# Performance work log

Hardware: AMD Instinct MI355X
Metric: run time of the kernel (lower is better)

## Reference

```python
import jax, jax.numpy as jnp
import numpy as np

N_USER = 100000
N_ITEM = 50000
D = 64
E_SOC = 3200000
E_INFO = 3200000
BATCH = 16384


def setup_inputs() -> dict:
    key = jax.random.key(0)
    ks = jax.random.split(key, 8)
    return {
        "user_emb": jax.random.normal(ks[0], (N_USER, D), dtype=jnp.float32) * 0.01,
        "item_emb": jax.random.normal(ks[1], (N_ITEM, D), dtype=jnp.float32) * 0.01,
        "social_rows": jax.random.randint(ks[2], (E_SOC,), 0, N_USER, dtype=jnp.int32),
        "social_cols": jax.random.randint(ks[3], (E_SOC,), 0, N_USER, dtype=jnp.int32),
        "social_vals": jnp.ones((E_SOC,), dtype=jnp.float32),
        "info_rows": jax.random.randint(ks[4], (E_INFO,), 0, N_USER, dtype=jnp.int32),
        "info_cols": jax.random.randint(ks[5], (E_INFO,), 0, N_ITEM, dtype=jnp.int32),
        "info_vals": jnp.ones((E_INFO,), dtype=jnp.float32),
        "user_ids": jax.random.randint(ks[6], (BATCH,), 0, N_USER, dtype=jnp.int32),
        "item_ids": jax.random.randint(ks[7], (BATCH,), 0, N_ITEM, dtype=jnp.int32),
    }


def _spmm(rows, cols, vals, feats, n_rows):
    # (A @ feats) where A is COO [n_rows, n_cols]: gather, weight, scatter-add.
    msgs = vals[:, None] * feats[cols]  # [E, D]
    return jax.ops.segment_sum(msgs, rows, num_segments=n_rows)


def reference(user_emb, item_emb, social_rows, social_cols, social_vals,
              info_rows, info_cols, info_vals, user_ids, item_ids):
    n_user = user_emb.shape[0]
    eps = 1e-8

    # user embedding from items: D_info^{-1} * info_adj @ item_emb
    deg_info = jax.ops.segment_sum(info_vals, info_rows, num_segments=n_user) + eps
    user_from_items = _spmm(info_rows, info_cols, info_vals, item_emb, n_user) / deg_info[:, None]

    # two GCN layers over social graph: H' = D^{-1} A H + H
    deg_soc = jax.ops.segment_sum(social_vals, social_rows, num_segments=n_user) + eps

    def gcn(h):
        return _spmm(social_rows, social_cols, social_vals, h, n_user) / deg_soc[:, None] + h

    h1 = gcn(user_emb)
    h2 = gcn(h1)
    final_user = h1 + h2 + user_from_items

    # final_item = item_emb + init_item_feature = 2 * item_emb
    final_item = 2.0 * item_emb

    u = final_user[user_ids]
    v = final_item[item_ids]
    return jax.nn.sigmoid(jnp.sum(u * v, axis=-1))
```

## Files before the change

kernel.cpp:

```cpp
#include <hip/hip_runtime.h>
#include <hip/hip_bf16.h>

#define BA 512
#define CHUNK_A 4096
#define PB 8
#define NBINS_MAX 512
#define CAPS 8800
#define NBINM_C 64
#define CPAD 16

__device__ __forceinline__ float bf2f(unsigned short u) {
    return __uint_as_float(((unsigned int)u) << 16);
}
__device__ __forceinline__ unsigned short f2bf(float f) {
    unsigned int x = __float_as_uint(f);
    return (unsigned short)((x + 0x7fffu + ((x >> 16) & 1u)) >> 16);
}
__device__ __forceinline__ void unpk(unsigned int u, float& lo, float& hi) {
    lo = __uint_as_float(u << 16);
    hi = __uint_as_float(u & 0xffff0000u);
}
__device__ __forceinline__ unsigned int pack2(float lo, float hi) {
    return (unsigned int)f2bf(lo) | ((unsigned int)f2bf(hi) << 16);
}


__global__ __launch_bounds__(256) void conv_mark_kernel(const float* __restrict__ a,
                                                        unsigned short* __restrict__ oa, long long na,
                                                        const float* __restrict__ b,
                                                        unsigned short* __restrict__ ob, long long nb,
                                                        const float* __restrict__ sv, int Es,
                                                        const float* __restrict__ iv, int Ei,
                                                        int* __restrict__ notOnes,
                                                        const int* __restrict__ ids,
                                                        int* __restrict__ mark,
                                                        int* __restrict__ mlist,
                                                        int* __restrict__ n_marked, int n,
                                                        int* __restrict__ curS, int nbinS,
                                                        int* __restrict__ curMI, int capS) {
    long long t = (long long)blockIdx.x * blockDim.x + threadIdx.x;
    long long i4 = t * 4;
    if (i4 < na) {
        float4 f = *(const float4*)&a[i4];
        ushort4 o = { f2bf(f.x), f2bf(f.y), f2bf(f.z), f2bf(f.w) };
        *(ushort4*)&oa[i4] = o;
    }
    if (i4 < nb) {
        float4 f = *(const float4*)&b[i4];
        ushort4 o = { f2bf(f.x), f2bf(f.y), f2bf(f.z), f2bf(f.w) };
        *(ushort4*)&ob[i4] = o;
    }
    if (i4 + 4 <= Es) {
        float4 v = *(const float4*)&sv[i4];
        if (v.x != 1.f || v.y != 1.f || v.z != 1.f || v.w != 1.f) atomicOr(notOnes, 1);
    } else if (i4 < Es) {
        for (long long k = i4; k < Es; ++k) if (sv[k] != 1.f) atomicOr(notOnes, 1);
    }
    if (i4 + 4 <= Ei) {
        float4 v = *(const float4*)&iv[i4];
        if (v.x != 1.f || v.y != 1.f || v.z != 1.f || v.w != 1.f) atomicOr(notOnes, 1);
    } else if (i4 < Ei) {
        for (long long k = i4; k < Ei; ++k) if (iv[k] != 1.f) atomicOr(notOnes, 1);
    }
    int i = (int)t;
    if (i < nbinS) curS[i * CPAD] = i * capS;
    if (i < NBINM_C) curMI[i * CPAD] = i * capS;
    if (i < n) {
        int u = ids[i];
        if (atomicCAS(&mark[u], 0, -1) == 0) {
            int m = atomicAdd(n_marked, 1);
            mlist[m] = u;
            mark[u] = m + 1;
        }
    }
}

__global__ __launch_bounds__(512) void partA_all(const int* __restrict__ notOnes,
                                                 const int* __restrict__ sr,
                                                 const int* __restrict__ sc,
                                                 const float* __restrict__ sv, int Es,
                                                 const int* __restrict__ ir,
                                                 const int* __restrict__ ic,
                                                 const float* __restrict__ iv, int Ei,
                                                 const int* __restrict__ mark,
                                                 int* __restrict__ curS,
                                                 int* __restrict__ bufS4, int2* __restrict__ bufS8,
                                                 int nbinS, int capS,
                                                 int* __restrict__ curMI,
                                                 int* __restrict__ bufMI4, int2* __restrict__ bufMI8) {
    __shared__ int hS[NBINS_MAX], gS[NBINS_MAX], lS[NBINS_MAX];
    __shared__ int hI[NBINM_C], gI[NBINM_C], lI[NBINM_C];
    const bool ones = (*notOnes == 0);
    int tid = threadIdx.x;
    int base = blockIdx.x * CHUNK_A;
    for (int b = tid; b < nbinS; b += BA) hS[b] = 0;
    if (tid < NBINM_C) hI[tid] = 0;

    int e0 = base + tid * 8;
    int rS[8], cS[8], mI[8], cI[8], rI[8];
    float vS[8], vI[8];
    int nS = (e0 < Es) ? min(8, Es - e0) : 0;
    int nI = (e0 < Ei) ? min(8, Ei - e0) : 0;
    if (nS == 8) {
        *(int4*)&rS[0] = *(const int4*)&sr[e0]; *(int4*)&rS[4] = *(const int4*)&sr[e0 + 4];
        *(int4*)&cS[0] = *(const int4*)&sc[e0]; *(int4*)&cS[4] = *(const int4*)&sc[e0 + 4];
        if (!ones) {
            *(float4*)&vS[0] = *(const float4*)&sv[e0];
            *(float4*)&vS[4] = *(const float4*)&sv[e0 + 4];
        }
    } else {
        #pragma unroll 8
        for (int k = 0; k < 8; ++k)
            if (k < nS) { rS[k] = sr[e0 + k]; cS[k] = sc[e0 + k]; vS[k] = ones ? 1.f : sv[e0 + k]; }
    }
    if (nI == 8) {
        *(int4*)&rI[0] = *(const int4*)&ir[e0]; *(int4*)&rI[4] = *(const int4*)&ir[e0 + 4];
        *(int4*)&cI[0] = *(const int4*)&ic[e0]; *(int4*)&cI[4] = *(const int4*)&ic[e0 + 4];
        if (!ones) {
            *(float4*)&vI[0] = *(const float4*)&iv[e0];
            *(float4*)&vI[4] = *(const float4*)&iv[e0 + 4];
        }
    } else {
        #pragma unroll 8
        for (int k = 0; k < 8; ++k)
            if (k < nI) { rI[k] = ir[e0 + k]; cI[k] = ic[e0 + k]; vI[k] = ones ? 1.f : iv[e0 + k]; }
    }
    #pragma unroll 8
    for (int k = 0; k < 8; ++k) mI[k] = (k < nI) ? mark[rI[k]] : 0;
    __syncthreads();

    #pragma unroll 8
    for (int k = 0; k < 8; ++k) if (k < nS) atomicAdd(&hS[rS[k] >> PB], 1);
    #pragma unroll 8
    for (int k = 0; k < 8; ++k) if (mI[k] > 0) atomicAdd(&hI[(mI[k] - 1) >> 8], 1);
    __syncthreads();

    for (int b = tid; b < nbinS; b += BA) {
        int h = hS[b]; gS[b] = h ? atomicAdd(&curS[b * CPAD], h) : 0; lS[b] = 0;
    }
    if (tid < NBINM_C) {
        int h = hI[tid]; gI[tid] = h ? atomicAdd(&curMI[tid * CPAD], h) : 0; lI[tid] = 0;
    }
    __syncthreads();

    #pragma unroll 8
    for (int k = 0; k < 8; ++k) {
        if (k < nS) {
            int r = rS[k];
            int b = r >> PB;
            int off = atomicAdd(&lS[b], 1);
            long long dst = (long long)gS[b] + off;
            if (dst < (long long)(b + 1) * capS) {
                int meta = ((r & 255) << 17) | cS[k];
                if (ones) bufS4[dst] = meta;
                else      bufS8[dst] = make_int2(meta, __float_as_int(vS[k]));
            }
        }
    }
    #pragma unroll 8
    for (int k = 0; k < 8; ++k) {
        if (mI[k] > 0) {
            int m = mI[k] - 1;
            int b = m >> 8;
            int off = atomicAdd(&lI[b], 1);
            long long dst = (long long)gI[b] + off;
            if (dst < (long long)(b + 1) * capS) {
                int meta = ((m & 255) << 17) | cI[k];
                if (ones) bufMI4[dst] = meta;
                else      bufMI8[dst] = make_int2(meta, __float_as_int(vI[k]));
            }
        }
    }
}

__global__ __launch_bounds__(512) void partB_sort(const int* __restrict__ notOnes,
                                                  const int* __restrict__ cur_in,
                                                  const int* __restrict__ buf4,
                                                  const int2* __restrict__ buf8,
                                                  int* __restrict__ csr4,
                                                  int2* __restrict__ csr8,
                                                  int2* __restrict__ rowptr2,
                                                  int n_rows_total, int cap) {
    int bin = blockIdx.x;
    int rows0 = bin << 8;
    int nrows = min(256, n_rows_total - rows0);
    __shared__ int cur[256], wsum[4];
    const bool ones = (*notOnes == 0);
    int tid = threadIdx.x;
    if (tid < 256) cur[tid] = 0;
    __syncthreads();
    int gstart = bin * cap;
    int gend = cur_in[bin * CPAD];
    if (gend > gstart + cap) gend = gstart + cap;
    int cnt = gend - gstart;
    if (ones) {
        for (int i = tid; i < cnt; i += 512) atomicAdd(&cur[buf4[gstart + i] >> 17], 1);
    } else {
        for (int i = tid; i < cnt; i += 512) atomicAdd(&cur[buf8[gstart + i].x >> 17], 1);
    }
    __syncthreads();
    int lane = tid & 63, wid = tid >> 6;
    int x = 0, v = 0;
    if (tid < 256) {
        x = cur[tid]; v = x;
        #pragma unroll
        for (int d = 1; d < 64; d <<= 1) { int y = __shfl_up(v, d); if (lane >= d) v += y; }
        if (lane == 63) wsum[wid] = v;
    }
    __syncthreads();
    if (tid == 0) {
        int s = 0;
        #pragma unroll
        for (int k = 0; k < 4; ++k) { int t = wsum[k]; wsum[k] = s; s += t; }
    }
    __syncthreads();
    if (tid < 256) {
        int excl = wsum[wid] + v - x;
        if (tid < nrows) rowptr2[rows0 + tid] = make_int2(gstart + excl, gstart + excl + x);
        cur[tid] = excl;
    }
    __syncthreads();
    if (ones) {
        for (int i = tid; i < cnt; i += 512) {
            int e = buf4[gstart + i];
            int p = atomicAdd(&cur[e >> 17], 1);
            csr4[gstart + p] = e & 0x1FFFF;
        }
    } else {
        for (int i = tid; i < cnt; i += 512) {
            int2 e = buf8[gstart + i];
            int p = atomicAdd(&cur[e.x >> 17], 1);
            csr8[gstart + p] = make_int2(e.x & 0x1FFFF, e.y);
        }
    }
}

__global__ __launch_bounds__(256) void gather1_kernel(const int* __restrict__ notOnes,
                                                      const int2* __restrict__ rowptr2,
                                                      const int* __restrict__ csr4,
                                                      const int2* __restrict__ csr8,
                                                      const unsigned short* __restrict__ ub,
                                                      unsigned short* __restrict__ hb,
                                                      int n_user) {
    int w = (int)((blockIdx.x * (long long)blockDim.x + threadIdx.x) >> 6);
    if (w >= n_user) return;
    int lane = threadIdx.x & 63;
    int sub = lane >> 3;
    int d8 = (lane & 7) << 3;
    int2 seg = rowptr2[w];
    float a0 = 0, a1 = 0, a2 = 0, a3 = 0, a4 = 0, a5 = 0, a6 = 0, a7 = 0, degs;
    if (*notOnes == 0) {
        for (int j = seg.x + sub; j < seg.y; j += 8) {
            int c = csr4[j];
            int4 q = *(const int4*)&ub[(long long)c * 64 + d8];
            float f0, f1, f2, f3, f4, f5, f6, f7;
            unpk(q.x, f0, f1); unpk(q.y, f2, f3); unpk(q.z, f4, f5); unpk(q.w, f6, f7);
            a0 += f0; a1 += f1; a2 += f2; a3 += f3;
            a4 += f4; a5 += f5; a6 += f6; a7 += f7;
        }
        degs = (float)(seg.y - seg.x);
    } else {
        degs = 0.f;
        for (int j = seg.x + sub; j < seg.y; j += 8) {
            int2 e = csr8[j];
            float vv = __int_as_float(e.y);
            int4 q = *(const int4*)&ub[(long long)(e.x) * 64 + d8];
            float f0, f1, f2, f3, f4, f5, f6, f7;
            unpk(q.x, f0, f1); unpk(q.y, f2, f3); unpk(q.z, f4, f5); unpk(q.w, f6, f7);
            a0 += vv * f0; a1 += vv * f1; a2 += vv * f2; a3 += vv * f3;
            a4 += vv * f4; a5 += vv * f5; a6 += vv * f6; a7 += vv * f7;
        }
        #pragma unroll
        for (int m = 8; m < 64; m <<= 1) degs += __shfl_xor(degs, m);
    }
    #pragma unroll
    for (int m = 8; m < 64; m <<= 1) {
        a0 += __shfl_xor(a0, m); a1 += __shfl_xor(a1, m);
        a2 += __shfl_xor(a2, m); a3 += __shfl_xor(a3, m);
        a4 += __shfl_xor(a4, m); a5 += __shfl_xor(a5, m);
        a6 += __shfl_xor(a6, m); a7 += __shfl_xor(a7, m);
    }
    if (sub == 0) {
        float inv = 1.0f / (degs + 1e-8f);
        int4 qe = *(const int4*)&ub[(long long)w * 64 + d8];
        float g0, g1, g2, g3, g4, g5, g6, g7;
        unpk(qe.x, g0, g1); unpk(qe.y, g2, g3); unpk(qe.z, g4, g5); unpk(qe.w, g6, g7);
        int4 o;
        o.x = (int)pack2(fmaf(a0, inv, g0), fmaf(a1, inv, g1));
        o.y = (int)pack2(fmaf(a2, inv, g2), fmaf(a3, inv, g3));
        o.z = (int)pack2(fmaf(a4, inv, g4), fmaf(a5, inv, g5));
        o.w = (int)pack2(fmaf(a6, inv, g6), fmaf(a7, inv, g7));
        *(int4*)&hb[(long long)w * 64 + d8] = o;
    }
}

__global__ __launch_bounds__(256) void accSI_kernel(const int* __restrict__ notOnes,
                                                    const int* __restrict__ mlist,
                                                    const int* __restrict__ n_marked,
                                                    const int2* __restrict__ rowptr2,
                                                    const int* __restrict__ csrS4,
                                                    const int2* __restrict__ csrS8,
                                                    const unsigned short* __restrict__ hb,
                                                    const int2* __restrict__ rowptrI2,
                                                    const int* __restrict__ csrI4,
                                                    const int2* __restrict__ csrI8,
                                                    const unsigned short* __restrict__ ib,
                                                    float* __restrict__ accF) {
    int w = (int)((blockIdx.x * (long long)blockDim.x + threadIdx.x) >> 6);
    if (w >= *n_marked) return;
    int lane = threadIdx.x & 63;
    int sub = lane >> 3;
    int d8 = (lane & 7) << 3;
    int r = mlist[w];

    float a0 = 0, a1 = 0, a2 = 0, a3 = 0, a4 = 0, a5 = 0, a6 = 0, a7 = 0, dS;
    float b0 = 0, b1 = 0, b2 = 0, b3 = 0, b4 = 0, b5 = 0, b6 = 0, b7 = 0, dI;
    int2 segS = rowptr2[r];
    int2 segI = rowptrI2[w];
    if (*notOnes == 0) {
        for (int j = segS.x + sub; j < segS.y; j += 8) {
            int c = csrS4[j];
            int4 q = *(const int4*)&hb[(long long)c * 64 + d8];
            float f0, f1, f2, f3, f4, f5, f6, f7;
            unpk(q.x, f0, f1); unpk(q.y, f2, f3); unpk(q.z, f4, f5); unpk(q.w, f6, f7);
            a0 += f0; a1 += f1; a2 += f2; a3 += f3;
            a4 += f4; a5 += f5; a6 += f6; a7 += f7;
        }
        for (int j = segI.x + sub; j < segI.y; j += 8) {
            int c = csrI4[j];
            int4 q = *(const int4*)&ib[(long long)c * 64 + d8];
            float f0, f1, f2, f3, f4, f5, f6, f7;
            unpk(q.x, f0, f1); unpk(q.y, f2, f3); unpk(q.z, f4, f5); unpk(q.w, f6, f7);
            b0 += f0; b1 += f1; b2 += f2; b3 += f3;
            b4 += f4; b5 += f5; b6 += f6; b7 += f7;
        }
        dS = (float)(segS.y - segS.x);
        dI = (float)(segI.y - segI.x);
    } else {
        dS = 0.f; dI = 0.f;
        for (int j = segS.x + sub; j < segS.y; j += 8) {
            int2 e = csrS8[j];
            float vv = __int_as_float(e.y);
            int4 q = *(const int4*)&hb[(long long)e.x * 64 + d8];
            float f0, f1, f2, f3, f4, f5, f6, f7;
            unpk(q.x, f0, f1); unpk(q.y, f2, f3); unpk(q.z, f4, f5); unpk(q.w, f6, f7);
            a0 += vv * f0; a1 += vv * f1; a2 += vv * f2; a3 += vv * f3;
            a4 += vv * f4; a5 += vv * f5; a6 += vv * f6; a7 += vv * f7;
            dS += vv;
        }
        for (int j = segI.x + sub; j < segI.y; j += 8) {
            int2 e = csrI8[j];
            float vv = __int_as_float(e.y);
            int4 q = *(const int4*)&ib[(long long)e.x * 64 + d8];
            float f0, f1, f2, f3, f4, f5, f6, f7;
            unpk(q.x, f0, f1); unpk(q.y, f2, f3); unpk(q.z, f4, f5); unpk(q.w, f6, f7);
            b0 += vv * f0; b1 += vv * f1; b2 += vv * f2; b3 += vv * f3;
            b4 += vv * f4; b5 += vv * f5; b6 += vv * f6; b7 += vv * f7;
            dI += vv;
        }
        #pragma unroll
        for (int m = 8; m < 64; m <<= 1) { dS += __shfl_xor(dS, m); dI += __shfl_xor(dI, m); }
    }
    #pragma unroll
    for (int m = 8; m < 64; m <<= 1) {
        a0 += __shfl_xor(a0, m); a1 += __shfl_xor(a1, m);
        a2 += __shfl_xor(a2, m); a3 += __shfl_xor(a3, m);
        a4 += __shfl_xor(a4, m); a5 += __shfl_xor(a5, m);
        a6 += __shfl_xor(a6, m); a7 += __shfl_xor(a7, m);
        b0 += __shfl_xor(b0, m); b1 += __shfl_xor(b1, m);
        b2 += __shfl_xor(b2, m); b3 += __shfl_xor(b3, m);
        b4 += __shfl_xor(b4, m); b5 += __shfl_xor(b5, m);
        b6 += __shfl_xor(b6, m); b7 += __shfl_xor(b7, m);
    }
    if (sub == 0) {
        float iS = 1.0f / (dS + 1e-8f);
        float iI = 1.0f / (dI + 1e-8f);
        long long base = (long long)w * 64 + d8;
        float4 o0 = { a0 * iS + b0 * iI, a1 * iS + b1 * iI, a2 * iS + b2 * iI, a3 * iS + b3 * iI };
        float4 o1 = { a4 * iS + b4 * iI, a5 * iS + b5 * iI, a6 * iS + b6 * iI, a7 * iS + b7 * iI };
        *(float4*)&accF[base] = o0;
        *(float4*)&accF[base + 4] = o1;
    }
}

__global__ __launch_bounds__(256) void dot_kernel(const unsigned short* __restrict__ hb,
                                                  const float* __restrict__ accF,
                                                  const unsigned short* __restrict__ ib,
                                                  const int* __restrict__ mark,
                                                  const int* __restrict__ uids,
                                                  const int* __restrict__ iids,
                                                  float* __restrict__ out, int batch) {
    int w = (int)((blockIdx.x * (long long)blockDim.x + threadIdx.x) >> 6);
    int lane = threadIdx.x & 63;
    if (w >= batch) return;
    int u = uids[w], it = iids[w];
    long long m = (long long)(mark[u] - 1);
    float uv = 2.0f * bf2f(hb[(long long)u * 64 + lane]) + accF[m * 64 + lane];
    float vv = 2.0f * bf2f(ib[(long long)it * 64 + lane]);
    float p = uv * vv;
    #pragma unroll
    for (int off = 32; off; off >>= 1) p += __shfl_xor(p, off);
    if (lane == 0) out[w] = 1.0f / (1.0f + __expf(-p));
}


extern "C" void kernel_launch(void* const* d_in, const int* in_sizes, int n_in,
                              void* d_out, int out_size, void* d_ws, size_t ws_size,
                              hipStream_t stream) {
    const float* user_emb  = (const float*)d_in[0];
    const float* item_emb  = (const float*)d_in[1];
    const int*   soc_rows  = (const int*)d_in[2];
    const int*   soc_cols  = (const int*)d_in[3];
    const float* soc_vals  = (const float*)d_in[4];
    const int*   info_rows = (const int*)d_in[5];
    const int*   info_cols = (const int*)d_in[6];
    const float* info_vals = (const float*)d_in[7];
    const int*   user_ids  = (const int*)d_in[8];
    const int*   item_ids  = (const int*)d_in[9];
    float*       out       = (float*)d_out;

    const int n_user = in_sizes[0] / 64;
    const int n_item = in_sizes[1] / 64;
    const int E_soc  = in_sizes[2];
    const int E_info = in_sizes[5];
    const int batch  = in_sizes[8];

    const int nbinS = (n_user + 255) >> PB;
    const int nbinM = (batch + 255) >> 8;
    int capS = (int)((long long)E_soc * 256 / n_user);
    capS = capS + capS / 16 + 96;
    if (capS > CAPS) capS = CAPS;

    char* p = (char*)d_ws;
    auto alloc = [&](size_t bytes) { char* q = p; p += (bytes + 255) & ~size_t(255); return q; };
    int* mark     = (int*)alloc(sizeof(int) * n_user);
    int* n_marked = (int*)alloc(sizeof(int) * 64);
    size_t zero_bytes = (size_t)(p - (char*)d_ws);
    int* notOnes = n_marked + 2;
    int*  mlist    = (int*)alloc(sizeof(int) * batch);
    int*  curSoc   = (int*)alloc(sizeof(int) * nbinS * CPAD);
    int*  curMI    = (int*)alloc(sizeof(int) * NBINM_C * CPAD);
    int2* bufSoc   = (int2*)alloc(sizeof(int2) * (size_t)nbinS * capS);
    int2* csrSoc   = (int2*)alloc(sizeof(int2) * (size_t)nbinS * capS);
    int2* rowptr2  = (int2*)alloc(sizeof(int2) * (size_t)n_user);
    int2* bufMI    = (int2*)alloc(sizeof(int2) * (size_t)nbinM * capS);
    int2* csrI     = (int2*)alloc(sizeof(int2) * (size_t)nbinM * capS);
    int2* rowptrI2 = (int2*)alloc(sizeof(int2) * (size_t)batch);
    unsigned short* ub = (unsigned short*)alloc(sizeof(short) * (size_t)n_user * 64);
    unsigned short* ib = (unsigned short*)alloc(sizeof(short) * (size_t)n_item * 64);
    unsigned short* hb = (unsigned short*)alloc(sizeof(short) * (size_t)n_user * 64);
    float* accF        = (float*)alloc(sizeof(float) * (size_t)batch * 64);
    (void)ws_size;

    hipMemsetAsync(d_ws, 0, zero_bytes, stream);

    const int B = 256;
    long long na = (long long)n_user * 64, nbm = (long long)n_item * 64;
    long long cmax = na > nbm ? na : nbm;
    if ((long long)E_soc > cmax) cmax = E_soc;
    if ((long long)E_info > cmax) cmax = E_info;
    long long c4 = (cmax + 3) / 4;
    conv_mark_kernel<<<(int)((c4 + B - 1) / B), B, 0, stream>>>(
        user_emb, ub, na, item_emb, ib, nbm,
        soc_vals, E_soc, info_vals, E_info, notOnes,
        user_ids, mark, mlist, n_marked, batch,
        curSoc, nbinS, curMI, capS);

    int Emax = max(E_soc, E_info);
    int gA = (Emax + CHUNK_A - 1) / CHUNK_A;
    partA_all<<<gA, BA, 0, stream>>>(notOnes,
                                     soc_rows, soc_cols, soc_vals, E_soc,
                                     info_rows, info_cols, info_vals, E_info,
                                     mark, curSoc, (int*)bufSoc, bufSoc, nbinS, capS,
                                     curMI, (int*)bufMI, bufMI);

    partB_sort<<<nbinS, 512, 0, stream>>>(notOnes, curSoc, (const int*)bufSoc, bufSoc,
                                          (int*)csrSoc, csrSoc, rowptr2, n_user, capS);
    partB_sort<<<nbinM, 512, 0, stream>>>(notOnes, curMI, (const int*)bufMI, bufMI,
                                          (int*)csrI, csrI, rowptrI2, batch, capS);

    long long t1 = (long long)n_user * 64;
    gather1_kernel<<<(int)((t1 + B - 1) / B), B, 0, stream>>>(notOnes, rowptr2,
                                                              (const int*)csrSoc, csrSoc,
                                                              ub, hb, n_user);

    long long t2 = (long long)batch * 64;
    accSI_kernel<<<(int)((t2 + B - 1) / B), B, 0, stream>>>(notOnes, mlist, n_marked,
                                                            rowptr2, (const int*)csrSoc, csrSoc, hb,
                                                            rowptrI2, (const int*)csrI, csrI, ib,
                                                            accF);

    dot_kernel<<<(int)((t2 + B - 1) / B), B, 0, stream>>>(hb, accF, ib, mark,
                                                          user_ids, item_ids, out, batch);
}
```

Measured before the change: 201.8 us.

## Widen social bins, fuse sort launches, and fuse accumulation with final dot

The binning kernel now uses 1024-thread blocks, 8192-edge chunks and 512-row social bins (PB=9), so there are half as many bins and fewer global cursor atomics. The two sort launches become one kernel that dispatches social and item bins by block index. The per-unique-user accumulation and the dot kernel are merged, so each batch entry recomputes its second-hop and item aggregates and forms the dot product directly, dropping the accF buffer and one launch. In exchange, duplicate user ids in the batch repeat the aggregation work, and larger bins mean more shared-memory atomic contention per block. The capacity clamp is also removed.

Measured after the change: 183.7 us. 9.0% less time.

```diff
diff --git a/kernel.cpp b/kernel.cpp
--- a/kernel.cpp
+++ b/kernel.cpp
@@ -1,11 +1,10 @@
 #include <hip/hip_runtime.h>
 #include <hip/hip_bf16.h>
 
-#define BA 512
-#define CHUNK_A 4096
-#define PB 8
-#define NBINS_MAX 512
-#define CAPS 8800
+#define BA 1024
+#define CHUNK_A 8192
+#define PB 9
+#define NBINS_MAX 256
 #define NBINM_C 64
 #define CPAD 16
 
@@ -75,25 +74,25 @@
     }
 }
 
-__global__ __launch_bounds__(512) void partA_all(const int* __restrict__ notOnes,
-                                                 const int* __restrict__ sr,
-                                                 const int* __restrict__ sc,
-                                                 const float* __restrict__ sv, int Es,
-                                                 const int* __restrict__ ir,
-                                                 const int* __restrict__ ic,
-                                                 const float* __restrict__ iv, int Ei,
-                                                 const int* __restrict__ mark,
-                                                 int* __restrict__ curS,
-                                                 int* __restrict__ bufS4, int2* __restrict__ bufS8,
-                                                 int nbinS, int capS,
-                                                 int* __restrict__ curMI,
-                                                 int* __restrict__ bufMI4, int2* __restrict__ bufMI8) {
+__global__ __launch_bounds__(1024) void partA_all(const int* __restrict__ notOnes,
+                                                  const int* __restrict__ sr,
+                                                  const int* __restrict__ sc,
+                                                  const float* __restrict__ sv, int Es,
+                                                  const int* __restrict__ ir,
+                                                  const int* __restrict__ ic,
+                                                  const float* __restrict__ iv, int Ei,
+                                                  const int* __restrict__ mark,
+                                                  int* __restrict__ curS,
+                                                  int* __restrict__ bufS4, int2* __restrict__ bufS8,
+                                                  int nbinS, int capS,
+                                                  int* __restrict__ curMI,
+                                                  int* __restrict__ bufMI4, int2* __restrict__ bufMI8) {
     __shared__ int hS[NBINS_MAX], gS[NBINS_MAX], lS[NBINS_MAX];
     __shared__ int hI[NBINM_C], gI[NBINM_C], lI[NBINM_C];
     const bool ones = (*notOnes == 0);
     int tid = threadIdx.x;
     int base = blockIdx.x * CHUNK_A;
-    for (int b = tid; b < nbinS; b += BA) hS[b] = 0;
+    if (tid < nbinS) hS[tid] = 0;
     if (tid < NBINM_C) hI[tid] = 0;
 
     int e0 = base + tid * 8;
@@ -135,8 +134,8 @@
     for (int k = 0; k < 8; ++k) if (mI[k] > 0) atomicAdd(&hI[(mI[k] - 1) >> 8], 1);
     __syncthreads();
 
-    for (int b = tid; b < nbinS; b += BA) {
-        int h = hS[b]; gS[b] = h ? atomicAdd(&curS[b * CPAD], h) : 0; lS[b] = 0;
+    if (tid < nbinS) {
+        int h = hS[tid]; gS[tid] = h ? atomicAdd(&curS[tid * CPAD], h) : 0; lS[tid] = 0;
     }
     if (tid < NBINM_C) {
         int h = hI[tid]; gI[tid] = h ? atomicAdd(&curMI[tid * CPAD], h) : 0; lI[tid] = 0;
@@ -151,7 +150,7 @@
             int off = atomicAdd(&lS[b], 1);
             long long dst = (long long)gS[b] + off;
             if (dst < (long long)(b + 1) * capS) {
-                int meta = ((r & 255) << 17) | cS[k];
+                int meta = ((r & ((1 << PB) - 1)) << 17) | cS[k];
                 if (ones) bufS4[dst] = meta;
                 else      bufS8[dst] = make_int2(meta, __float_as_int(vS[k]));
             }
@@ -173,64 +172,70 @@
     }
 }
 
-__global__ __launch_bounds__(512) void partB_sort(const int* __restrict__ notOnes,
-                                                  const int* __restrict__ cur_in,
-                                                  const int* __restrict__ buf4,
-                                                  const int2* __restrict__ buf8,
-                                                  int* __restrict__ csr4,
-                                                  int2* __restrict__ csr8,
-                                                  int2* __restrict__ rowptr2,
-                                                  int n_rows_total, int cap) {
+__global__ __launch_bounds__(512) void sort_fused(const int* __restrict__ notOnes,
+                                                  const int* __restrict__ curS,
+                                                  const int* __restrict__ bufS4, const int2* __restrict__ bufS8,
+                                                  int* __restrict__ csrS4, int2* __restrict__ csrS8,
+                                                  int2* __restrict__ rowptrS, int nbinS, int n_user,
+                                                  const int* __restrict__ curI,
+                                                  const int* __restrict__ bufI4, const int2* __restrict__ bufI8,
+                                                  int* __restrict__ csrI4, int2* __restrict__ csrI8,
+                                                  int2* __restrict__ rowptrI, int batch,
+                                                  int cap) {
+    __shared__ int cur[512], wsum[8];
+    const bool ones = (*notOnes == 0);
     int bin = blockIdx.x;
-    int rows0 = bin << 8;
-    int nrows = min(256, n_rows_total - rows0);
-    __shared__ int cur[256], wsum[4];
-    const bool ones = (*notOnes == 0);
+    const int* cin; const int* b4; const int2* b8;
+    int* c4; int2* c8; int2* rp;
+    int binL, rows0, ntot, rpb;
+    if (bin < nbinS) {
+        binL = bin; cin = curS; b4 = bufS4; b8 = bufS8; c4 = csrS4; c8 = csrS8;
+        rp = rowptrS; rows0 = binL << PB; ntot = n_user; rpb = 1 << PB;
+    } else {
+        binL = bin - nbinS; cin = curI; b4 = bufI4; b8 = bufI8; c4 = csrI4; c8 = csrI8;
+        rp = rowptrI; rows0 = binL << 8; ntot = batch; rpb = 256;
+    }
     int tid = threadIdx.x;
-    if (tid < 256) cur[tid] = 0;
-    __syncthreads();
-    int gstart = bin * cap;
-    int gend = cur_in[bin * CPAD];
+    cur[tid] = 0;
+    __syncthreads();
+    long long gstart = (long long)binL * cap;
+    long long gend = cin[binL * CPAD];
     if (gend > gstart + cap) gend = gstart + cap;
-    int cnt = gend - gstart;
+    int cnt = (int)(gend - gstart);
     if (ones) {
-        for (int i = tid; i < cnt; i += 512) atomicAdd(&cur[buf4[gstart + i] >> 17], 1);
-    } else {
-        for (int i = tid; i < cnt; i += 512) atomicAdd(&cur[buf8[gstart + i].x >> 17], 1);
+        for (int i = tid; i < cnt; i += 512) atomicAdd(&cur[b4[gstart + i] >> 17], 1);
+    } else {
+        for (int i = tid; i < cnt; i += 512) atomicAdd(&cur[b8[gstart + i].x >> 17], 1);
     }
     __syncthreads();
     int lane = tid & 63, wid = tid >> 6;
-    int x = 0, v = 0;
-    if (tid < 256) {
-        x = cur[tid]; v = x;
-        #pragma unroll
-        for (int d = 1; d < 64; d <<= 1) { int y = __shfl_up(v, d); if (lane >= d) v += y; }
-        if (lane == 63) wsum[wid] = v;
-    }
+    int x = cur[tid], v = x;
+    #pragma unroll
+    for (int d = 1; d < 64; d <<= 1) { int y = __shfl_up(v, d); if (lane >= d) v += y; }
+    if (lane == 63) wsum[wid] = v;
     __syncthreads();
     if (tid == 0) {
         int s = 0;
         #pragma unroll
-        for (int k = 0; k < 4; ++k) { int t = wsum[k]; wsum[k] = s; s += t; }
-    }
-    __syncthreads();
-    if (tid < 256) {
-        int excl = wsum[wid] + v - x;
-        if (tid < nrows) rowptr2[rows0 + tid] = make_int2(gstart + excl, gstart + excl + x);
-        cur[tid] = excl;
-    }
+        for (int k = 0; k < 8; ++k) { int t = wsum[k]; wsum[k] = s; s += t; }
+    }
+    __syncthreads();
+    int excl = wsum[wid] + v - x;
+    int nrows = min(rpb, ntot - rows0);
+    if (tid < nrows) rp[rows0 + tid] = make_int2((int)gstart + excl, (int)gstart + excl + x);
+    cur[tid] = excl;
     __syncthreads();
     if (ones) {
         for (int i = tid; i < cnt; i += 512) {
-            int e = buf4[gstart + i];
-            int p = atomicAdd(&cur[e >> 17], 1);
-            csr4[gstart + p] = e & 0x1FFFF;
+            int e = b4[gstart + i];
+            int p2 = atomicAdd(&cur[e >> 17], 1);
+            c4[gstart + p2] = e & 0x1FFFF;
         }
     } else {
         for (int i = tid; i < cnt; i += 512) {
-            int2 e = buf8[gstart + i];
-            int p = atomicAdd(&cur[e.x >> 17], 1);
-            csr8[gstart + p] = make_int2(e.x & 0x1FFFF, e.y);
+            int2 e = b8[gstart + i];
+            int p2 = atomicAdd(&cur[e.x >> 17], 1);
+            c8[gstart + p2] = make_int2(e.x & 0x1FFFF, e.y);
         }
     }
 }
@@ -294,9 +299,7 @@
     }
 }
 
-__global__ __launch_bounds__(256) void accSI_kernel(const int* __restrict__ notOnes,
-                                                    const int* __restrict__ mlist,
-                                                    const int* __restrict__ n_marked,
+__global__ __launch_bounds__(256) void dotSI_kernel(const int* __restrict__ notOnes,
                                                     const int2* __restrict__ rowptr2,
                                                     const int* __restrict__ csrS4,
                                                     const int2* __restrict__ csrS8,
@@ -305,18 +308,22 @@
                                                     const int* __restrict__ csrI4,
                                                     const int2* __restrict__ csrI8,
                                                     const unsigned short* __restrict__ ib,
-                                                    float* __restrict__ accF) {
+                                                    const int* __restrict__ mark,
+                                                    const int* __restrict__ uids,
+                                                    const int* __restrict__ iids,
+                                                    float* __restrict__ out, int batch) {
     int w = (int)((blockIdx.x * (long long)blockDim.x + threadIdx.x) >> 6);
-    if (w >= *n_marked) return;
+    if (w >= batch) return;
     int lane = threadIdx.x & 63;
     int sub = lane >> 3;
     int d8 = (lane & 7) << 3;
-    int r = mlist[w];
+    int u = uids[w], it = iids[w];
+    int m = mark[u] - 1;
 
     float a0 = 0, a1 = 0, a2 = 0, a3 = 0, a4 = 0, a5 = 0, a6 = 0, a7 = 0, dS;
     float b0 = 0, b1 = 0, b2 = 0, b3 = 0, b4 = 0, b5 = 0, b6 = 0, b7 = 0, dI;
-    int2 segS = rowptr2[r];
-    int2 segI = rowptrI2[w];
+    int2 segS = rowptr2[u];
+    int2 segI = rowptrI2[m];
     if (*notOnes == 0) {
         for (int j = segS.x + sub; j < segS.y; j += 8) {
             int c = csrS4[j];
@@ -359,47 +366,36 @@
             dI += vv;
         }
         #pragma unroll
-        for (int m = 8; m < 64; m <<= 1) { dS += __shfl_xor(dS, m); dI += __shfl_xor(dI, m); }
+        for (int mm = 8; mm < 64; mm <<= 1) { dS += __shfl_xor(dS, mm); dI += __shfl_xor(dI, mm); }
     }
     #pragma unroll
-    for (int m = 8; m < 64; m <<= 1) {
-        a0 += __shfl_xor(a0, m); a1 += __shfl_xor(a1, m);
-        a2 += __shfl_xor(a2, m); a3 += __shfl_xor(a3, m);
-        a4 += __shfl_xor(a4, m); a5 += __shfl_xor(a5, m);
-        a6 += __shfl_xor(a6, m); a7 += __shfl_xor(a7, m);
-        b0 += __shfl_xor(b0, m); b1 += __shfl_xor(b1, m);
-        b2 += __shfl_xor(b2, m); b3 += __shfl_xor(b3, m);
-        b4 += __shfl_xor(b4, m); b5 += __shfl_xor(b5, m);
-        b6 += __shfl_xor(b6, m); b7 += __shfl_xor(b7, m);
-    }
-    if (sub == 0) {
-        float iS = 1.0f / (dS + 1e-8f);
-        float iI = 1.0f / (dI + 1e-8f);
-        long long base = (long long)w * 64 + d8;
-        float4 o0 = { a0 * iS + b0 * iI, a1 * iS + b1 * iI, a2 * iS + b2 * iI, a3 * iS + b3 * iI };
-        float4 o1 = { a4 * iS + b4 * iI, a5 * iS + b5 * iI, a6 * iS + b6 * iI, a7 * iS + b7 * iI };
-        *(float4*)&accF[base] = o0;
-        *(float4*)&accF[base + 4] = o1;
-    }
-}
-
-__global__ __launch_bounds__(256) void dot_kernel(const unsigned short* __restrict__ hb,
-                                                  const float* __restrict__ accF,
-                                                  const unsigned short* __restrict__ ib,
-                                                  const int* __restrict__ mark,
-                                                  const int* __restrict__ uids,
-                                                  const int* __restrict__ iids,
-                                                  float* __restrict__ out, int batch) {
-    int w = (int)((blockIdx.x * (long long)blockDim.x + threadIdx.x) >> 6);
-    int lane = threadIdx.x & 63;
-    if (w >= batch) return;
-    int u = uids[w], it = iids[w];
-    long long m = (long long)(mark[u] - 1);
-    float uv = 2.0f * bf2f(hb[(long long)u * 64 + lane]) + accF[m * 64 + lane];
-    float vv = 2.0f * bf2f(ib[(long long)it * 64 + lane]);
-    float p = uv * vv;
-    #pragma unroll
-    for (int off = 32; off; off >>= 1) p += __shfl_xor(p, off);
+    for (int mm = 8; mm < 64; mm <<= 1) {
+        a0 += __shfl_xor(a0, mm); a1 += __shfl_xor(a1, mm);
+        a2 += __shfl_xor(a2, mm); a3 += __shfl_xor(a3, mm);
+        a4 += __shfl_xor(a4, mm); a5 += __shfl_xor(a5, mm);
+        a6 += __shfl_xor(a6, mm); a7 += __shfl_xor(a7, mm);
+        b0 += __shfl_xor(b0, mm); b1 += __shfl_xor(b1, mm);
+        b2 += __shfl_xor(b2, mm); b3 += __shfl_xor(b3, mm);
+        b4 += __shfl_xor(b4, mm); b5 += __shfl_xor(b5, mm);
+        b6 += __shfl_xor(b6, mm); b7 += __shfl_xor(b7, mm);
+    }
+    float iS = 1.0f / (dS + 1e-8f);
+    float iI = 1.0f / (dI + 1e-8f);
+    int4 qh = *(const int4*)&hb[(long long)u * 64 + d8];
+    int4 qi = *(const int4*)&ib[(long long)it * 64 + d8];
+    float h0, h1, h2, h3, h4, h5, h6, h7;
+    float t0, t1, t2, t3, t4, t5, t6, t7;
+    unpk(qh.x, h0, h1); unpk(qh.y, h2, h3); unpk(qh.z, h4, h5); unpk(qh.w, h6, h7);
+    unpk(qi.x, t0, t1); unpk(qi.y, t2, t3); unpk(qi.z, t4, t5); unpk(qi.w, t6, t7);
+    float p = (2.f * h0 + a0 * iS + b0 * iI) * (2.f * t0)
+            + (2.f * h1 + a1 * iS + b1 * iI) * (2.f * t1)
+            + (2.f * h2 + a2 * iS + b2 * iI) * (2.f * t2)
+            + (2.f * h3 + a3 * iS + b3 * iI) * (2.f * t3)
+            + (2.f * h4 + a4 * iS + b4 * iI) * (2.f * t4)
+            + (2.f * h5 + a5 * iS + b5 * iI) * (2.f * t5)
+            + (2.f * h6 + a6 * iS + b6 * iI) * (2.f * t6)
+            + (2.f * h7 + a7 * iS + b7 * iI) * (2.f * t7);
+    p += __shfl_xor(p, 1); p += __shfl_xor(p, 2); p += __shfl_xor(p, 4);
     if (lane == 0) out[w] = 1.0f / (1.0f + __expf(-p));
 }
 
@@ -425,11 +421,10 @@
     const int E_info = in_sizes[5];
     const int batch  = in_sizes[8];
 
-    const int nbinS = (n_user + 255) >> PB;
+    const int nbinS = (n_user + (1 << PB) - 1) >> PB;
     const int nbinM = (batch + 255) >> 8;
-    int capS = (int)((long long)E_soc * 256 / n_user);
-    capS = capS + capS / 16 + 96;
-    if (capS > CAPS) capS = CAPS;
+    int capS = (int)((long long)E_soc * (1 << PB) / n_user);
+    capS = capS + capS / 16 + 128;
 
     char* p = (char*)d_ws;
     auto alloc = [&](size_t bytes) { char* q = p; p += (bytes + 255) & ~size_t(255); return q; };
@@ -449,7 +444,6 @@
     unsigned short* ub = (unsigned short*)alloc(sizeof(short) * (size_t)n_user * 64);
     unsigned short* ib = (unsigned short*)alloc(sizeof(short) * (size_t)n_item * 64);
     unsigned short* hb = (unsigned short*)alloc(sizeof(short) * (size_t)n_user * 64);
-    float* accF        = (float*)alloc(sizeof(float) * (size_t)batch * 64);
     (void)ws_size;
 
     hipMemsetAsync(d_ws, 0, zero_bytes, stream);
@@ -474,10 +468,11 @@
                                      mark, curSoc, (int*)bufSoc, bufSoc, nbinS, capS,
                                      curMI, (int*)bufMI, bufMI);
 
-    partB_sort<<<nbinS, 512, 0, stream>>>(notOnes, curSoc, (const int*)bufSoc, bufSoc,
-                                          (int*)csrSoc, csrSoc, rowptr2, n_user, capS);
-    partB_sort<<<nbinM, 512, 0, stream>>>(notOnes, curMI, (const int*)bufMI, bufMI,
-                                          (int*)csrI, csrI, rowptrI2, batch, capS);
+    sort_fused<<<nbinS + nbinM, 512, 0, stream>>>(notOnes,
+                                                  curSoc, (const int*)bufSoc, bufSoc,
+                                                  (int*)csrSoc, csrSoc, rowptr2, nbinS, n_user,
+                                                  curMI, (const int*)bufMI, bufMI,
+                                                  (int*)csrI, csrI, rowptrI2, batch, capS);
 
     long long t1 = (long long)n_user * 64;
     gather1_kernel<<<(int)((t1 + B - 1) / B), B, 0, stream>>>(notOnes, rowptr2,
@@ -485,11 +480,8 @@
                                                               ub, hb, n_user);
 
     long long t2 = (long long)batch * 64;
-    accSI_kernel<<<(int)((t2 + B - 1) / B), B, 0, stream>>>(notOnes, mlist, n_marked,
+    dotSI_kernel<<<(int)((t2 + B - 1) / B), B, 0, stream>>>(notOnes,
                                                             rowptr2, (const int*)csrSoc, csrSoc, hb,
                                                             rowptrI2, (const int*)csrI, csrI, ib,
-                                                            accF);
-
-    dot_kernel<<<(int)((t2 + B - 1) / B), B, 0, stream>>>(hb, accF, ib, mark,
-                                                          user_ids, item_ids, out, batch);
-}
+                                                            mark, user_ids, item_ids, out, batch);
+}
```
